# Kernel optimization log

Measured on AMD Instinct MI355X. Metric: run time of the kernel, lower is better.

The kernel has to match this reference:

```python
import jax, jax.numpy as jnp
import numpy as np

N_NODES = 100
F_IN = 65536
C_OUT = 60
ACTION_DIM = 100
N_EDGES = 2000


def setup_inputs() -> dict:
    key = jax.random.key(0)
    ks = jax.random.split(key, 16)
    s = 0.02
    return {
        "substrate_features": jax.random.normal(ks[0], (1, N_NODES, F_IN), jnp.float32),
        "edge_index": jax.random.randint(ks[1], (2, N_EDGES), 0, N_NODES, dtype=jnp.int32),
        "v_cpu_demand_t": jax.random.uniform(ks[2], (1,), jnp.float32),
        "v_bw_demand_t": jax.random.uniform(ks[3], (1,), jnp.float32),
        "num_pending_v_nodes_t": jax.random.uniform(ks[4], (1,), jnp.float32),
        "actor_w": jax.random.normal(ks[5], (3, F_IN, C_OUT), jnp.float32) * s,
        "actor_b": jax.random.normal(ks[6], (C_OUT,), jnp.float32) * s,
        "critic_w": jax.random.normal(ks[7], (3, F_IN, C_OUT), jnp.float32) * s,
        "critic_b": jax.random.normal(ks[8], (C_OUT,), jnp.float32) * s,
        "actor_fc_w": jax.random.normal(ks[9], (N_NODES * C_OUT + 3, ACTION_DIM), jnp.float32) * s,
        "actor_fc_b": jax.random.normal(ks[10], (ACTION_DIM,), jnp.float32) * s,
        "critic_fc_w": jax.random.normal(ks[11], (N_NODES * C_OUT + 3, 1), jnp.float32) * s,
        "critic_fc_b": jax.random.normal(ks[12], (1,), jnp.float32) * s,
    }


def cheb_conv(x, edge_index, W, b):
    # ChebConv, K=3, sym normalization, lambda_max=2 (PyG defaults).
    # With lambda_max=2 the scaled Laplacian is L_hat = -D^{-1/2} A D^{-1/2}
    # (diagonal becomes 0 after the -1 self-loop shift).
    # x: [1, N, F]; edge_index: [2, E]; W: [3, F, C]; b: [C]
    src, dst = edge_index[0], edge_index[1]
    n = x.shape[1]
    deg = jax.ops.segment_sum(jnp.ones(src.shape[0], x.dtype), src, num_segments=n)
    dis = jnp.where(deg > 0, jax.lax.rsqrt(jnp.where(deg > 0, deg, 1.0)), 0.0)
    norm = -(dis[src] * dis[dst])  # [E], L_hat off-diagonal entries
    x2 = x[0]  # [N, F]

    def prop(z):  # z: [N, F] -> L_hat @ z via gather/scatter over edges
        return jax.ops.segment_sum(z[src] * norm[:, None], dst, num_segments=n)

    Tx0 = x2
    Tx1 = prop(Tx0)
    Tx2 = 2.0 * prop(Tx1) - Tx0
    out = Tx0 @ W[0] + Tx1 @ W[1] + Tx2 @ W[2] + b  # [N, C]
    return out[None]  # [1, N, C]


def reference(substrate_features, edge_index, v_cpu_demand_t, v_bw_demand_t,
              num_pending_v_nodes_t, actor_w, actor_b, critic_w, critic_b,
              actor_fc_w, actor_fc_b, critic_fc_w, critic_fc_b):
    emb_a = jnp.tanh(cheb_conv(substrate_features, edge_index, actor_w, actor_b))
    emb_a = emb_a.reshape(1, -1)  # [1, N*60]
    emb_c = jnp.tanh(cheb_conv(substrate_features, edge_index, critic_w, critic_b))
    emb_c = emb_c.reshape(1, -1)
    extras = [v_cpu_demand_t[None], v_bw_demand_t[None], num_pending_v_nodes_t[None]]  # each [1,1]
    state_a = jnp.concatenate([emb_a] + extras, axis=1)  # [1, 6003]
    state_c = jnp.concatenate([emb_c] + extras, axis=1)
    logits = state_a @ actor_fc_w + actor_fc_b  # [1, action_dim]
    values = state_c @ critic_fc_w + critic_fc_b  # [1, 1]
    return (logits, values)
```

## Files before the change

kernel.cpp:

```cpp
#include <hip/hip_runtime.h>
#include <stdint.h>

#define F_IN 65536
#define NN 100
#define CO 60
#define G_SPLIT 128
#define KC (F_IN/G_SPLIT)
#define BK 64
#define NIT (KC/BK)
#define AST 72

typedef short v8s __attribute__((ext_vector_type(8)));
typedef float v4f __attribute__((ext_vector_type(4)));

__device__ __forceinline__ unsigned int f2bf(float x){
  unsigned int u = __float_as_uint(x);
  u += 0x7fffu + ((u>>16)&1u);
  return u>>16;
}

__device__ __forceinline__ v4f mfma16(v8s a, v8s b, v4f c){
  return __builtin_amdgcn_mfma_f32_16x16x32_bf16(a,b,c,0,0,0);
}

__global__ __launch_bounds__(256,2)
void k_gemm(const float* __restrict__ x, const float* __restrict__ aw,
            const float* __restrict__ cw, float* __restrict__ dst, int partial){
  const int s  = blockIdx.x;
  const int g  = blockIdx.y;
  const int k0 = s*KC;
  const int tid = threadIdx.x;
  const int wave = tid>>6, lane = tid&63, quad = lane>>4, nl = lane&15;
  const int c0 = wave*16;
  const int ccl = min(c0+nl, CO-1);

  const float* W  = (g<3) ? (aw + (size_t)g*F_IN*CO) : (cw + (size_t)(g-3)*F_IN*CO);
  const float* wp = W + (size_t)(k0 + quad*8)*CO + ccl;

  __shared__ __align__(16) unsigned short Al[2][112*AST];

  float4 ra[7];
  float  rb[16];
  #pragma unroll
  for(int p=0;p<7;++p){
    int lin = p*256 + tid, row = lin>>4, q = lin&15;
    int rcl = min(row, NN-1);
    ra[p] = *(const float4*)(x + (size_t)rcl*F_IN + k0 + q*4);
  }
  #pragma unroll
  for(int u=0;u<16;++u) rb[u] = wp[((u>>3)*32 + (u&7))*CO];

  v4f acc[7];
  #pragma unroll
  for(int i=0;i<7;++i){ v4f z={0.f,0.f,0.f,0.f}; acc[i]=z; }

  for(int it=0; it<NIT; ++it){
    unsigned short* buf = Al[it&1];
    #pragma unroll
    for(int p=0;p<7;++p){
      int lin = p*256 + tid, row = lin>>4, q = lin&15;
      uint2 w;
      w.x = f2bf(ra[p].x) | (f2bf(ra[p].y)<<16);
      w.y = f2bf(ra[p].z) | (f2bf(ra[p].w)<<16);
      *(uint2*)(buf + row*AST + q*4) = w;
    }
    v8s fB0, fB1;
    #pragma unroll
    for(int j=0;j<8;++j){
      fB0[j] = (short)f2bf(rb[j]);
      fB1[j] = (short)f2bf(rb[8+j]);
    }
    __syncthreads();
    if(it+1 < NIT){
      const int kb = k0 + (it+1)*BK;
      #pragma unroll
      for(int p=0;p<7;++p){
        int lin = p*256 + tid, row = lin>>4, q = lin&15;
        int rcl = min(row, NN-1);
        ra[p] = *(const float4*)(x + (size_t)rcl*F_IN + kb + q*4);
      }
      #pragma unroll
      for(int u=0;u<16;++u) rb[u] = wp[((it+1)*BK + (u>>3)*32 + (u&7))*CO];
    }
    #pragma unroll
    for(int mt=0; mt<7; ++mt){
      const unsigned short* arow = buf + (mt*16+nl)*AST + quad*8;
      v8s a0 = *(const v8s*)(arow);
      v8s a1 = *(const v8s*)(arow+32);
      acc[mt] = mfma16(a0, fB0, acc[mt]);
      acc[mt] = mfma16(a1, fB1, acc[mt]);
    }
  }

  const int c = c0 + nl;
  if(c < CO){
    if(partial){
      float* pd = dst + ((size_t)g*G_SPLIT + s)*(NN*CO);
      #pragma unroll
      for(int mt=0;mt<7;++mt){
        #pragma unroll
        for(int i=0;i<4;++i){
          int m = mt*16 + quad*4 + i;
          if(m < NN) pd[m*CO + c] = acc[mt][i];
        }
      }
    } else {
      float* pd = dst + (size_t)g*(NN*CO);
      #pragma unroll
      for(int mt=0;mt<7;++mt){
        #pragma unroll
        for(int i=0;i<4;++i){
          int m = mt*16 + quad*4 + i;
          if(m < NN) atomicAdd(pd + m*CO + c, acc[mt][i]);
        }
      }
    }
  }
}

__global__ void k_reduce(const float* __restrict__ P, float* __restrict__ Y){
  int o = blockIdx.x*256 + threadIdx.x;
  if(o >= 6*NN*CO) return;
  int gg = o/(NN*CO), r = o - gg*(NN*CO);
  const float* p = P + (size_t)gg*G_SPLIT*(NN*CO) + (size_t)blockIdx.y*32*(NN*CO) + r;
  float a0=0.f,a1=0.f,a2=0.f,a3=0.f;
  #pragma unroll 2
  for(int s4=0;s4<32;s4+=4){
    a0 += p[(s4  )*(NN*CO)];
    a1 += p[(s4+1)*(NN*CO)];
    a2 += p[(s4+2)*(NN*CO)];
    a3 += p[(s4+3)*(NN*CO)];
  }
  atomicAdd(&Y[o], (a0+a1)+(a2+a3));
}

__global__ void k_cheb(const float* __restrict__ Y, const int* __restrict__ ei,
                       const float* __restrict__ ab, const float* __restrict__ cb,
                       float* __restrict__ emb){
  const int net = blockIdx.x / CO;
  const int c   = blockIdx.x % CO;
  const int t   = threadIdx.x;
  __shared__ float L[NN][NN+1];
  __shared__ float dis[NN];
  __shared__ int   deg[NN];
  __shared__ float y0[NN], y1[NN], y2[NN], zu[NN];

  for(int i=t;i<NN*(NN+1);i+=128) ((float*)L)[i]=0.f;
  if(t<NN) deg[t]=0;
  __syncthreads();
  for(int e=t;e<2000;e+=128) atomicAdd(&deg[ei[e]],1);
  __syncthreads();
  if(t<NN) dis[t] = deg[t]>0 ? rsqrtf((float)deg[t]) : 0.f;
  __syncthreads();
  for(int e=t;e<2000;e+=128){
    int s = ei[e], d = ei[2000+e];
    atomicAdd(&L[d][s], -dis[s]*dis[d]);
  }
  if(t<NN){
    const float* yb = Y + (size_t)net*3*NN*CO + t*CO + c;
    y0[t]=yb[0]; y1[t]=yb[NN*CO]; y2[t]=yb[2*NN*CO];
  }
  __syncthreads();
  if(t<NN){
    float s=0.f;
    #pragma unroll 4
    for(int j=0;j<NN;++j) s += L[t][j]*y2[j];
    zu[t] = y1[t] + 2.f*s;
  }
  __syncthreads();
  if(t<NN){
    float s=0.f;
    #pragma unroll 4
    for(int j=0;j<NN;++j) s += L[t][j]*zu[j];
    float b = (net==0) ? ab[c] : cb[c];
    emb[net*NN*CO + t*CO + c] = tanhf(y0[t] - y2[t] + s + b);
  }
}

#define FCB 25
__global__ void k_fc(const float* __restrict__ emb, const float* __restrict__ afw,
                     const float* __restrict__ afb, const float* __restrict__ cfw,
                     const float* __restrict__ cfb, const float* __restrict__ s0,
                     const float* __restrict__ s1, const float* __restrict__ s2,
                     float* __restrict__ out){
  const int b = blockIdx.x;
  const int t = threadIdx.x;
  if(b < FCB){
    const int jj = t & 127, half = t >> 7;
    if(jj < 100){
      const int i0 = b*240 + half*120;
      const float* w = afw + (size_t)i0*100 + jj;
      const float* e = emb + i0;
      float p = 0.f;
      #pragma unroll 4
      for(int i=0;i<120;++i) p += e[i]*w[(size_t)i*100];
      atomicAdd(&out[jj], p);
    }
  } else {
    float p = 0.f;
    const float* e = emb + 6000;
    for(int i=t;i<6000;i+=256) p += e[i]*cfw[i];
    #pragma unroll
    for(int o=32;o>0;o>>=1) p += __shfl_down(p,o,64);
    __shared__ float red[4];
    if((t&63)==0) red[t>>6]=p;
    __syncthreads();
    if(t==0){
      float tot = red[0]+red[1]+red[2]+red[3];
      out[100] = tot + s0[0]*cfw[6000] + s1[0]*cfw[6001] + s2[0]*cfw[6002] + cfb[0];
    }
    if(t<100){
      atomicAdd(&out[t], afb[t] + s0[0]*afw[600000+t] + s1[0]*afw[600100+t] + s2[0]*afw[600200+t]);
    }
  }
}

extern "C" void kernel_launch(void* const* d_in, const int* in_sizes, int n_in,
                              void* d_out, int out_size, void* d_ws, size_t ws_size,
                              hipStream_t stream){
  const float* x   = (const float*)d_in[0];
  const int*   ei  = (const int*)d_in[1];
  const float* s0  = (const float*)d_in[2];
  const float* s1  = (const float*)d_in[3];
  const float* s2  = (const float*)d_in[4];
  const float* aw  = (const float*)d_in[5];
  const float* ab  = (const float*)d_in[6];
  const float* cw  = (const float*)d_in[7];
  const float* cb  = (const float*)d_in[8];
  const float* afw = (const float*)d_in[9];
  const float* afb = (const float*)d_in[10];
  const float* cfw = (const float*)d_in[11];
  const float* cfb = (const float*)d_in[12];
  float* out = (float*)d_out;

  float* Y   = (float*)d_ws;
  float* emb = Y + 6*NN*CO;
  float* P   = emb + 2*NN*CO;
  const size_t need = (size_t)(6*NN*CO + 2*NN*CO + (size_t)6*G_SPLIT*NN*CO)*sizeof(float);
  const int partial = (ws_size >= need) ? 1 : 0;

  hipMemsetAsync(Y, 0, 6*NN*CO*sizeof(float), stream);
  hipMemsetAsync(out, 0, 101*sizeof(float), stream);

  k_gemm<<<dim3(G_SPLIT,6), 256, 0, stream>>>(x, aw, cw, partial ? P : Y, partial);
  if(partial){
    k_reduce<<<dim3((6*NN*CO+255)/256, 4), 256, 0, stream>>>(P, Y);
  }
  k_cheb<<<120, 128, 0, stream>>>(Y, ei, ab, cb, emb);
  k_fc<<<FCB+1, 256, 0, stream>>>(emb, afw, afb, cfw, cfb, s0, s1, s2, out);
}
```

Measured before the change: 216.6 us.

## Stage weight tiles through LDS, remap blocks per XCD, and drop memsets

The GEMM kernel now loads each weight tile with coalesced float4 reads, converts it to bf16 into a double-buffered LDS tile, and builds the MFMA B fragments from LDS. Previously each lane did strided scalar global reads. Blocks are launched on a 1D grid and remapped so that consecutive K-slices of all six weight matrices land on the same XCD, and launch bounds are raised to 3 blocks per SM. The reduce kernel now sums all partials in a single pass and writes Y directly instead of using atomics. The Y and out memsets are removed, with the output zeroing moved into the cheb kernel. The extra LDS and the higher occupancy target may pressure registers, and the single-pass reduce has less parallelism.

```diff
diff --git a/kernel.cpp b/kernel.cpp
--- a/kernel.cpp
+++ b/kernel.cpp
@@ -9,6 +9,8 @@
 #define BK 64
 #define NIT (KC/BK)
 #define AST 72
+#define BTILE (BK*CO)
+#define BQ (BTILE/4)
 
 typedef short v8s __attribute__((ext_vector_type(8)));
 typedef float v4f __attribute__((ext_vector_type(4)));
@@ -23,24 +25,28 @@
   return __builtin_amdgcn_mfma_f32_16x16x32_bf16(a,b,c,0,0,0);
 }
 
-__global__ __launch_bounds__(256,2)
+__global__ __launch_bounds__(256,3)
 void k_gemm(const float* __restrict__ x, const float* __restrict__ aw,
             const float* __restrict__ cw, float* __restrict__ dst, int partial){
-  const int s  = blockIdx.x;
-  const int g  = blockIdx.y;
-  const int k0 = s*KC;
-  const int tid = threadIdx.x;
+  const int bid  = blockIdx.x;
+  const int xcd  = bid & 7, slot = bid >> 3;
+  const int sdiv = slot / 6;
+  const int s    = xcd*16 + sdiv;
+  const int g    = slot - sdiv*6;
+  const int k0   = s*KC;
+  const int tid  = threadIdx.x;
   const int wave = tid>>6, lane = tid&63, quad = lane>>4, nl = lane&15;
-  const int c0 = wave*16;
-  const int ccl = min(c0+nl, CO-1);
-
-  const float* W  = (g<3) ? (aw + (size_t)g*F_IN*CO) : (cw + (size_t)(g-3)*F_IN*CO);
-  const float* wp = W + (size_t)(k0 + quad*8)*CO + ccl;
+  const int c0   = wave*16;
+  const int ccl  = min(c0+nl, CO-1);
+
+  const float* W    = (g<3) ? (aw + (size_t)g*F_IN*CO) : (cw + (size_t)(g-3)*F_IN*CO);
+  const float* bsrc = W + (size_t)k0*CO;
 
   __shared__ __align__(16) unsigned short Al[2][112*AST];
+  __shared__ __align__(16) unsigned short Bl[2][BTILE];
 
   float4 ra[7];
-  float  rb[16];
+  float4 rbv[4];
   #pragma unroll
   for(int p=0;p<7;++p){
     int lin = p*256 + tid, row = lin>>4, q = lin&15;
@@ -48,14 +54,18 @@
     ra[p] = *(const float4*)(x + (size_t)rcl*F_IN + k0 + q*4);
   }
   #pragma unroll
-  for(int u=0;u<16;++u) rb[u] = wp[((u>>3)*32 + (u&7))*CO];
+  for(int p=0;p<4;++p){
+    int f = min(p*256 + tid, BQ-1);
+    rbv[p] = *(const float4*)(bsrc + f*4);
+  }
 
   v4f acc[7];
   #pragma unroll
   for(int i=0;i<7;++i){ v4f z={0.f,0.f,0.f,0.f}; acc[i]=z; }
 
   for(int it=0; it<NIT; ++it){
-    unsigned short* buf = Al[it&1];
+    unsigned short* buf  = Al[it&1];
+    unsigned short* bbuf = Bl[it&1];
     #pragma unroll
     for(int p=0;p<7;++p){
       int lin = p*256 + tid, row = lin>>4, q = lin&15;
@@ -64,11 +74,15 @@
       w.y = f2bf(ra[p].z) | (f2bf(ra[p].w)<<16);
       *(uint2*)(buf + row*AST + q*4) = w;
     }
-    v8s fB0, fB1;
-    #pragma unroll
-    for(int j=0;j<8;++j){
-      fB0[j] = (short)f2bf(rb[j]);
-      fB1[j] = (short)f2bf(rb[8+j]);
+    #pragma unroll
+    for(int p=0;p<4;++p){
+      int f = p*256 + tid;
+      if(f < BQ){
+        uint2 w;
+        w.x = f2bf(rbv[p].x) | (f2bf(rbv[p].y)<<16);
+        w.y = f2bf(rbv[p].z) | (f2bf(rbv[p].w)<<16);
+        *(uint2*)(bbuf + f*4) = w;
+      }
     }
     __syncthreads();
     if(it+1 < NIT){
@@ -79,8 +93,19 @@
         int rcl = min(row, NN-1);
         ra[p] = *(const float4*)(x + (size_t)rcl*F_IN + kb + q*4);
       }
-      #pragma unroll
-      for(int u=0;u<16;++u) rb[u] = wp[((it+1)*BK + (u>>3)*32 + (u&7))*CO];
+      const float* bs2 = bsrc + (size_t)(it+1)*BK*CO;
+      #pragma unroll
+      for(int p=0;p<4;++p){
+        int f = min(p*256 + tid, BQ-1);
+        rbv[p] = *(const float4*)(bs2 + f*4);
+      }
+    }
+    const unsigned short* bb = bbuf + quad*8*CO + ccl;
+    v8s fB0, fB1;
+    #pragma unroll
+    for(int j=0;j<8;++j){
+      fB0[j] = (short)bb[j*CO];
+      fB1[j] = (short)bb[32*CO + j*CO];
     }
     #pragma unroll
     for(int mt=0; mt<7; ++mt){
@@ -122,21 +147,21 @@
   int o = blockIdx.x*256 + threadIdx.x;
   if(o >= 6*NN*CO) return;
   int gg = o/(NN*CO), r = o - gg*(NN*CO);
-  const float* p = P + (size_t)gg*G_SPLIT*(NN*CO) + (size_t)blockIdx.y*32*(NN*CO) + r;
+  const float* p = P + (size_t)gg*G_SPLIT*(NN*CO) + r;
   float a0=0.f,a1=0.f,a2=0.f,a3=0.f;
-  #pragma unroll 2
-  for(int s4=0;s4<32;s4+=4){
-    a0 += p[(s4  )*(NN*CO)];
-    a1 += p[(s4+1)*(NN*CO)];
-    a2 += p[(s4+2)*(NN*CO)];
-    a3 += p[(s4+3)*(NN*CO)];
-  }
-  atomicAdd(&Y[o], (a0+a1)+(a2+a3));
+  #pragma unroll 4
+  for(int s4=0;s4<G_SPLIT;s4+=4){
+    a0 += p[(size_t)(s4  )*(NN*CO)];
+    a1 += p[(size_t)(s4+1)*(NN*CO)];
+    a2 += p[(size_t)(s4+2)*(NN*CO)];
+    a3 += p[(size_t)(s4+3)*(NN*CO)];
+  }
+  Y[o] = (a0+a1)+(a2+a3);
 }
 
 __global__ void k_cheb(const float* __restrict__ Y, const int* __restrict__ ei,
                        const float* __restrict__ ab, const float* __restrict__ cb,
-                       float* __restrict__ emb){
+                       float* __restrict__ emb, float* __restrict__ out){
   const int net = blockIdx.x / CO;
   const int c   = blockIdx.x % CO;
   const int t   = threadIdx.x;
@@ -144,6 +169,8 @@
   __shared__ float dis[NN];
   __shared__ int   deg[NN];
   __shared__ float y0[NN], y1[NN], y2[NN], zu[NN];
+
+  if(blockIdx.x==0 && t<101) out[t] = 0.f;
 
   for(int i=t;i<NN*(NN+1);i+=128) ((float*)L)[i]=0.f;
   if(t<NN) deg[t]=0;
@@ -239,13 +266,13 @@
   const size_t need = (size_t)(6*NN*CO + 2*NN*CO + (size_t)6*G_SPLIT*NN*CO)*sizeof(float);
   const int partial = (ws_size >= need) ? 1 : 0;
 
-  hipMemsetAsync(Y, 0, 6*NN*CO*sizeof(float), stream);
-  hipMemsetAsync(out, 0, 101*sizeof(float), stream);
-
-  k_gemm<<<dim3(G_SPLIT,6), 256, 0, stream>>>(x, aw, cw, partial ? P : Y, partial);
   if(partial){
-    k_reduce<<<dim3((6*NN*CO+255)/256, 4), 256, 0, stream>>>(P, Y);
-  }
-  k_cheb<<<120, 128, 0, stream>>>(Y, ei, ab, cb, emb);
+    k_gemm<<<dim3(G_SPLIT*6), 256, 0, stream>>>(x, aw, cw, P, 1);
+    k_reduce<<<dim3((6*NN*CO+255)/256), 256, 0, stream>>>(P, Y);
+  } else {
+    hipMemsetAsync(Y, 0, 6*NN*CO*sizeof(float), stream);
+    k_gemm<<<dim3(G_SPLIT*6), 256, 0, stream>>>(x, aw, cw, Y, 0);
+  }
+  k_cheb<<<120, 128, 0, stream>>>(Y, ei, ab, cb, emb, out);
   k_fc<<<FCB+1, 256, 0, stream>>>(emb, afw, afb, cfw, cfb, s0, s1, s2, out);
 }
```

Result: no change. 213.5 us (-1.4%).
